# Kernel tuning notes

Measured on AMD Instinct MI355X. Metric: run time of the kernel, lower is better.

Reference implementation:

```python
import jax, jax.numpy as jnp
import numpy as np

B, L, S = 128, 80, 8          # dialogues, utterances per dialogue, speakers
NODE_DIM, HIDDEN, HEADS, OUT_DIM = 768, 512, 8, 256
N = B * L


def _build_edges():
    """Replicates InterSentenceGNN.build_graph + Batch.from_data_list offsets."""
    rel = np.zeros((N, 3), np.float32)
    all_e, last = [], []
    eye3 = np.eye(3, dtype=np.float32)
    for b in range(B):
        off = b * L
        u = L - 1
        e, t = [], []
        for i in range(L):
            if i > 0:
                e += [[i - 1, i], [i, i - 1]]; t += [0, 0]   # REL_SEQ
            if i < u:
                e += [[i, u], [u, i]]; t += [1, 1]           # REL_CTX
        for s in range(S):                                   # REL_SPK, round-robin speakers
            g = list(range(s, L, S))
            for a in range(len(g)):
                for c in range(a + 1, len(g)):
                    e += [[g[a], g[c]], [g[c], g[a]]]; t += [2, 2]
        e = np.asarray(e, np.int64); t = np.asarray(t, np.int64)
        np.add.at(rel, e[:, 0] + off, eye3[t])               # out-degree per relation (pre-unique)
        all_e.append(np.unique(e, axis=0) + off)             # torch.unique(idx, dim=1)
        last.append(off + u)
    edge_index = np.concatenate(all_e, 0).T.astype(np.int32)  # [2, E], row0=src, row1=dst
    return edge_index, rel, np.asarray(last, np.int32)


def setup_inputs() -> dict:
    key = jax.random.key(0)
    ks = jax.random.split(key, 16)
    edge_index, rel_feat, last_idx = _build_edges()
    g = lambda k, shp, fan: jax.random.normal(k, shp, jnp.float32) * (1.0 / np.sqrt(fan))
    return {
        "x": jax.random.normal(ks[0], (N, NODE_DIM), jnp.float32),
        "rel_feat": jnp.asarray(rel_feat),
        "w1": g(ks[1], (3, 64), 3), "b1": jnp.zeros((64,), jnp.float32),
        "w2": g(ks[2], (64, 1), 64), "b2": jnp.zeros((1,), jnp.float32),
        "Wl1": g(ks[3], (NODE_DIM, HIDDEN), NODE_DIM), "bl1": jnp.zeros((HIDDEN,), jnp.float32),
        "Wr1": g(ks[4], (NODE_DIM, HIDDEN), NODE_DIM), "br1": jnp.zeros((HIDDEN,), jnp.float32),
        "att1": g(ks[5], (HEADS, HIDDEN // HEADS), HIDDEN // HEADS),
        "bias1": jnp.zeros((HIDDEN,), jnp.float32),
        "Wl2": g(ks[6], (HIDDEN, OUT_DIM), HIDDEN), "bl2": jnp.zeros((OUT_DIM,), jnp.float32),
        "Wr2": g(ks[7], (HIDDEN, OUT_DIM), HIDDEN), "br2": jnp.zeros((OUT_DIM,), jnp.float32),
        "att2": g(ks[8], (1, OUT_DIM), OUT_DIM),
        "bias2": jnp.zeros((OUT_DIM,), jnp.float32),
        "ln_g": jnp.ones((OUT_DIM,), jnp.float32), "ln_b": jnp.zeros((OUT_DIM,), jnp.float32),
        "edge_index": jnp.asarray(edge_index),
        "last_idx": jnp.asarray(last_idx),
    }


def _gatv2(x, Wl, bl, Wr, br, att, bias, src, dst, heads, ch, concat):
    """PyG GATv2Conv (eval mode, self-loops already in src/dst)."""
    n = x.shape[0]
    xl = (x @ Wl + bl).reshape(n, heads, ch)   # source transform (messages)
    xr = (x @ Wr + br).reshape(n, heads, ch)   # target transform
    e = jax.nn.leaky_relu(xl[src] + xr[dst], negative_slope=0.2)  # [E,H,C]
    logit = jnp.einsum("ehc,hc->eh", e, att)                      # [E,H]
    m = jax.ops.segment_max(logit, dst, num_segments=n)
    a = jnp.exp(logit - m[dst])
    denom = jax.ops.segment_sum(a, dst, num_segments=n)
    alpha = a / denom[dst]                                        # segment softmax over dst
    msg = (xl[src] * alpha[:, :, None]).reshape(-1, heads * ch)
    out = jax.ops.segment_sum(msg, dst, num_segments=n).reshape(n, heads, ch)
    out = out.reshape(n, heads * ch) if concat else out.mean(axis=1)
    return out + bias


def reference(x, rel_feat, w1, b1, w2, b2, Wl1, bl1, Wr1, br1, att1, bias1,
              Wl2, bl2, Wr2, br2, att2, bias2, ln_g, ln_b, edge_index, last_idx):
    n = x.shape[0]
    loops = jnp.arange(n, dtype=edge_index.dtype)
    src = jnp.concatenate([edge_index[0], loops])  # add_self_loops=True (PyG default)
    dst = jnp.concatenate([edge_index[1], loops])
    w = jax.nn.sigmoid(jax.nn.relu(rel_feat @ w1 + b1) @ w2 + b2)  # [N,1] node gate
    h = x * w
    h = jax.nn.elu(_gatv2(h, Wl1, bl1, Wr1, br1, att1, bias1, src, dst, HEADS, HIDDEN // HEADS, True))
    h = _gatv2(h, Wl2, bl2, Wr2, br2, att2, bias2, src, dst, 1, OUT_DIM, False)
    mu = jnp.mean(h, axis=-1, keepdims=True)
    var = jnp.mean((h - mu) ** 2, axis=-1, keepdims=True)
    h = (h - mu) * jax.lax.rsqrt(var + 1e-5) * ln_g + ln_b
    return h[last_idx]  # x[batch.ptr[1:] - 1]: last (context) node per dialogue
```

## Files before the change

kernel.cpp:

```cpp
#include <hip/hip_runtime.h>
#include <hip/hip_bf16.h>

#define NN 10240
#define LL 80
#define BB 128

typedef _Float16 half8 __attribute__((ext_vector_type(8)));
typedef _Float16 half2v __attribute__((ext_vector_type(2)));
typedef float f32x4 __attribute__((ext_vector_type(4)));

#define GLD16(gptr, lptr)                                                        \
  __builtin_amdgcn_global_load_lds(                                              \
      (const __attribute__((address_space(1))) void*)(gptr),                     \
      (__attribute__((address_space(3))) void*)(lptr), 16, 0, 0)

__device__ __forceinline__ float dot2f(half2v a, half2v b, float c) {
#if __has_builtin(__builtin_amdgcn_fdot2)
  return __builtin_amdgcn_fdot2(a, b, c, false);
#else
  return c + (float)a.x * (float)b.x + (float)a.y * (float)b.y;
#endif
}
__device__ __forceinline__ half2v u2h(unsigned int u) { half2v r; __builtin_memcpy(&r, &u, 4); return r; }
__device__ __forceinline__ unsigned int h2u(half2v h) { unsigned int u; __builtin_memcpy(&u, &h, 4); return u; }
__device__ __forceinline__ unsigned int dupf16(float v) {
  _Float16 hv = (_Float16)v;
  unsigned short u; __builtin_memcpy(&u, &hv, 2);
  return (unsigned int)u * 0x10001u;
}
__device__ __forceinline__ int roff(int r) { return r * 66 + 4 * (r >> 3); }

__global__ __launch_bounds__(256) void prep_all(
    const float* __restrict__ x, const float* __restrict__ rel,
    const float* __restrict__ w1, const float* __restrict__ b1,
    const float* __restrict__ w2, const float* __restrict__ b2,
    const float* __restrict__ Wl1, const float* __restrict__ Wr1,
    const float* __restrict__ Wl2, const float* __restrict__ Wr2,
    const float* __restrict__ bl1, const float* __restrict__ br1,
    const float* __restrict__ att1,
    _Float16* __restrict__ h0, _Float16* __restrict__ Wt1,
    _Float16* __restrict__ Wt2cat,
    float* __restrict__ biasc, _Float16* __restrict__ att_h) {
  __shared__ float tile[32][33];
  int bid = blockIdx.x;
  int tid = threadIdx.x;
  if (bid < NN) {
    int n = bid;
    __shared__ float s_w;
    if (tid < 64) {
      float r0 = rel[n * 3 + 0], r1 = rel[n * 3 + 1], r2 = rel[n * 3 + 2];
      float v = r0 * w1[tid] + r1 * w1[64 + tid] + r2 * w1[128 + tid] + b1[tid];
      v = v > 0.f ? v : 0.f;
      v *= w2[tid];
      for (int d = 32; d; d >>= 1) v += __shfl_down(v, d, 64);
      if (tid == 0) s_w = 1.f / (1.f + __expf(-(v + b2[0])));
    }
    __syncthreads();
    float w = s_w;
    const float* xr = x + (size_t)n * 768;
    _Float16* hr = h0 + (size_t)n * 768;
    for (int c = tid; c < 768; c += 256) hr[c] = (_Float16)(xr[c] * w);
    return;
  }
  int r = bid - NN;
  const float* W;
  _Float16* Wt;
  int K, Nc, bx, by;
  if (r < 384)      { W = Wl1; Wt = Wt1;                          K = 768; Nc = 512; bx = r % 16;       by = r / 16; }
  else if (r < 768) { W = Wr1; Wt = Wt1 + (size_t)512 * 768;      K = 768; Nc = 512; bx = (r-384) % 16; by = (r-384) / 16; }
  else if (r < 896) { W = Wl2; Wt = Wt2cat;                       K = 512; Nc = 256; bx = (r-768) % 8;  by = (r-768) / 8; }
  else if (r < 1024){ W = Wr2; Wt = Wt2cat + (size_t)256 * 512;   K = 512; Nc = 256; bx = (r-896) % 8;  by = (r-896) / 8; }
  else {
    for (int i = tid; i < 1024; i += 256) biasc[i] = (i < 512) ? bl1[i] : br1[i - 512];
    for (int i = tid; i < 512; i += 256) att_h[i] = (_Float16)att1[i];
    return;
  }
  int n0 = bx * 32, k0 = by * 32;
  int c = tid & 31, rr = tid >> 5;
#pragma unroll
  for (int p = 0; p < 4; ++p) {
    int rw = p * 8 + rr;
    tile[rw][c] = W[(size_t)(k0 + rw) * Nc + n0 + c];
  }
  __syncthreads();
#pragma unroll
  for (int p = 0; p < 4; ++p) {
    int rw = p * 8 + rr;
    Wt[(size_t)(n0 + rw) * K + k0 + c] = (_Float16)tile[c][rw];
  }
}

__global__ __launch_bounds__(512, 8) void gemm1gat1(
    const _Float16* __restrict__ h0, const _Float16* __restrict__ Wt1,
    const float* __restrict__ biasc, const _Float16* __restrict__ att_h,
    const float* __restrict__ bias1, _Float16* __restrict__ h1) {
  __shared__ __align__(16) char smem[39936];
  _Float16* As = (_Float16*)smem;
  _Float16* Bs = (_Float16*)(smem + 15360);
  _Float16* s_xl = (_Float16*)smem;
  _Float16* s_xr = (_Float16*)(smem + 10640);
  float* s_logit = (float*)(smem + 21280);
  unsigned int* s_al = (unsigned int*)(smem + 26464);
  short* s_src   = (short*)(smem + 31648);
  short* s_cnt   = (short*)(smem + 34240);
  float* s_hub   = (float*)(smem + 34400);
  unsigned int* s_hub16 = (unsigned int*)(smem + 34720);
  unsigned int* s_hp = (unsigned int*)(smem + 35040);

  int bx = blockIdx.x;
  int h = bx >> 7, b = bx & 127;
  int base = b * LL;
  int tid = threadIdx.x;
  int wave = tid >> 6, lane = tid & 63;
  int lr = lane & 15, lk = lane >> 4;

  int seg8 = ((lane & 3) ^ ((lane >> 3) & 3)) * 8;
  const _Float16* aP = h0;
  if (wave < 5) {
    int c = wave * 64 + lane;
    aP = h0 + (size_t)(base + (c >> 2)) * 768 + seg8;
  }
  int cB = wave * 64 + lane;
  int brow = cB >> 2;
  int wrow = (brow < 64) ? (h * 64 + brow) : (512 + h * 64 + (brow - 64));
  const _Float16* bP = Wt1 + (size_t)wrow * 768 + seg8;

  int xk8 = (lk ^ ((lr >> 1) & 3)) * 8;

  f32x4 acc[5] = {};
  for (int it = 0; it < 8; ++it) {
    int k0 = it * 96;
    if (wave < 5) {
      GLD16(aP + k0,      As + wave * 512);
      GLD16(aP + k0 + 32, As + 2560 + wave * 512);
      GLD16(aP + k0 + 64, As + 5120 + wave * 512);
    }
    GLD16(bP + k0,      Bs + wave * 512);
    GLD16(bP + k0 + 32, Bs + 4096 + wave * 512);
    GLD16(bP + k0 + 64, Bs + 8192 + wave * 512);
    __syncthreads();
#pragma unroll
    for (int s3 = 0; s3 < 3; ++s3) {
      half8 bf = *(const half8*)(Bs + s3 * 4096 + (wave * 16 + lr) * 32 + xk8);
#pragma unroll
      for (int m = 0; m < 5; ++m) {
        half8 af = *(const half8*)(As + s3 * 2560 + (m * 16 + lr) * 32 + xk8);
        acc[m] = __builtin_amdgcn_mfma_f32_16x16x32_f16(af, bf, acc[m], 0, 0, 0);
      }
    }
    __syncthreads();
  }
  {
    int c = wave * 16 + lr;
    bool isxl = c < 64;
    int cc = isxl ? c : c - 64;
    float bb = biasc[(isxl ? 0 : 512) + h * 64 + cc];
    _Float16* dst = isxl ? s_xl : s_xr;
#pragma unroll
    for (int m = 0; m < 5; ++m)
#pragma unroll
      for (int rg = 0; rg < 4; ++rg) {
        int row = m * 16 + lk * 4 + rg;
        dst[roff(row) + cc] = (_Float16)(acc[m][rg] + bb);
      }
  }
  if (tid < 79) {
    int d = tid;
    int list[16];
    int c = 0;
    list[c++] = d;
    if (d > 0) list[c++] = d - 1;
    if (d + 1 < 79) list[c++] = d + 1;
    list[c++] = 79;
    for (int j = d & 7; j < 80; j += 8)
      if (j != d && j != 79) list[c++] = j;
    s_cnt[d] = (short)c;
    for (int i = c; i < 16; ++i) list[i] = -1;
#pragma unroll
    for (int i = 0; i < 16; ++i) s_src[i * 81 + d] = (short)list[i];
  }
  __syncthreads();

  const unsigned int* pat = (const unsigned int*)(att_h + h * 64);
  const half2v c02 = {(_Float16)0.2f, (_Float16)0.2f};
  for (int s = tid; s < 1344; s += 512) {
    int d, src;
    bool ishub = s >= 1264;
    if (!ishub) { d = s >> 4; src = s_src[(s & 15) * 81 + d]; }
    else { d = 79; src = s - 1264; }
    int ssrc = src < 0 ? 0 : src;
    const unsigned int* pa = (const unsigned int*)(s_xl + roff(ssrc));
    const unsigned int* pb = (const unsigned int*)(s_xr + roff(d));
    float acc2 = 0.f;
#pragma unroll
    for (int q = 0; q < 16; ++q) {
      unsigned int a0 = pa[2 * q], a1 = pa[2 * q + 1];
      unsigned int b0 = pb[2 * q], b1 = pb[2 * q + 1];
      half2v at0 = u2h(__builtin_amdgcn_readfirstlane(pat[2 * q]));
      half2v at1 = u2h(__builtin_amdgcn_readfirstlane(pat[2 * q + 1]));
      half2v e0 = u2h(a0) + u2h(b0);
      half2v e1 = u2h(a1) + u2h(b1);
      half2v l0 = __builtin_elementwise_max(e0, e0 * c02);
      half2v l1 = __builtin_elementwise_max(e1, e1 * c02);
      acc2 = dot2f(l0, at0, acc2);
      acc2 = dot2f(l1, at1, acc2);
    }
    if (!ishub) s_logit[(s & 15) * 81 + d] = (src < 0) ? -3e38f : acc2;
    else s_hub[src] = acc2;
  }
  __syncthreads();

  if (tid < 79) {
    int d = tid;
    float m = -3e38f, v[16];
#pragma unroll
    for (int i = 0; i < 16; ++i) { v[i] = s_logit[i * 81 + d]; m = fmaxf(m, v[i]); }
    float sum = 0.f;
#pragma unroll
    for (int i = 0; i < 16; ++i) { v[i] = __expf(v[i] - m); sum += v[i]; }
    float inv = 1.f / sum;
#pragma unroll
    for (int i = 0; i < 16; ++i) s_al[i * 81 + d] = dupf16(v[i] * inv);
  } else if (tid >= 448) {
    int l = tid - 448;
    float v0 = s_hub[l];
    float v1 = (l < 16) ? s_hub[64 + l] : -3e38f;
    float m = fmaxf(v0, v1);
    for (int d = 32; d; d >>= 1) m = fmaxf(m, __shfl_xor(m, d, 64));
    float e0 = __expf(v0 - m);
    float e1 = (l < 16) ? __expf(v1 - m) : 0.f;
    float sum = e0 + e1;
    for (int d = 32; d; d >>= 1) sum += __shfl_xor(sum, d, 64);
    float inv = 1.f / sum;
    s_hub16[l] = dupf16(e0 * inv);
    if (l < 16) s_hub16[64 + l] = dupf16(e1 * inv);
  }
  __syncthreads();

  int qw = tid >> 4, l = tid & 15;
  int c0 = l * 4;
#pragma unroll
  for (int k = 0; k < 3; ++k) {
    int d = qw + 32 * k;
    if (d >= 79) continue;
    int cnt = s_cnt[d];
    half2v a0 = {(_Float16)0.f, (_Float16)0.f};
    half2v a1 = a0;
    for (int i = 0; i < cnt; ++i) {
      int src = s_src[i * 81 + d];
      half2v al = u2h(s_al[i * 81 + d]);
      const unsigned int* px = (const unsigned int*)(s_xl + roff(src) + c0);
      a0 += al * u2h(px[0]);
      a1 += al * u2h(px[1]);
    }
    float v0 = (float)a0.x + bias1[h * 64 + c0];
    float v1 = (float)a0.y + bias1[h * 64 + c0 + 1];
    float v2 = (float)a1.x + bias1[h * 64 + c0 + 2];
    float v3 = (float)a1.y + bias1[h * 64 + c0 + 3];
    v0 = v0 > 0.f ? v0 : __expf(v0) - 1.f;
    v1 = v1 > 0.f ? v1 : __expf(v1) - 1.f;
    v2 = v2 > 0.f ? v2 : __expf(v2) - 1.f;
    v3 = v3 > 0.f ? v3 : __expf(v3) - 1.f;
    half2v o0 = {(_Float16)v0, (_Float16)v1};
    half2v o1 = {(_Float16)v2, (_Float16)v3};
    uint2 ov = {h2u(o0), h2u(o1)};
    *(uint2*)&h1[(size_t)(base + d) * 512 + h * 64 + c0] = ov;
  }
  if (qw >= 16) {
    int g = qw - 16;
    half2v a0 = {(_Float16)0.f, (_Float16)0.f};
    half2v a1 = a0;
#pragma unroll
    for (int s5 = 0; s5 < 5; ++s5) {
      int src = g * 5 + s5;
      half2v al = u2h(s_hub16[src]);
      const unsigned int* px = (const unsigned int*)(s_xl + roff(src) + c0);
      a0 += al * u2h(px[0]);
      a1 += al * u2h(px[1]);
    }
    s_hp[g * 32 + 2 * l] = h2u(a0);
    s_hp[g * 32 + 2 * l + 1] = h2u(a1);
  }
  __syncthreads();
  if (tid < 32) {
    float f0 = 0.f, f1 = 0.f;
#pragma unroll
    for (int g = 0; g < 16; ++g) {
      half2v v = u2h(s_hp[g * 32 + tid]);
      f0 += (float)v.x;
      f1 += (float)v.y;
    }
    int c = tid * 2;
    float v0 = f0 + bias1[h * 64 + c];
    float v1 = f1 + bias1[h * 64 + c + 1];
    v0 = v0 > 0.f ? v0 : __expf(v0) - 1.f;
    v1 = v1 > 0.f ? v1 : __expf(v1) - 1.f;
    half2v o = {(_Float16)v0, (_Float16)v1};
    *(unsigned int*)&h1[(size_t)(base + 79) * 512 + h * 64 + c] = h2u(o);
  }
}

#define PX 266
__global__ __launch_bounds__(512) void gemm2gat2(
    const _Float16* __restrict__ h1, const _Float16* __restrict__ Bt,
    const float* __restrict__ bl2, const float* __restrict__ br2,
    const float* __restrict__ att2, const float* __restrict__ bias2,
    const float* __restrict__ ln_g, const float* __restrict__ ln_b,
    float* __restrict__ out) {
  __shared__ __align__(16) char smem[80 * PX * 2];
  __shared__ _Float16 s_att[256];
  __shared__ _Float16 s_xr[256];
  __shared__ float s_red[80];
  __shared__ float s_sum[4], s_sq[4];
  _Float16* As = (_Float16*)smem;
  _Float16* Bs = (_Float16*)(smem + 5120);
  _Float16* s_x = (_Float16*)smem;

  int b = blockIdx.x;
  int tid = threadIdx.x;
  int wave = tid >> 6, lane = tid & 63;
  int lr = lane & 15, lk = lane >> 4;

  if (tid < 256) s_att[tid] = (_Float16)att2[tid];

  int seg8 = ((lane & 3) ^ ((lane >> 3) & 3)) * 8;
  int achunk = wave * 64 + lane;
  const _Float16* aP = h1 + (size_t)(b * 80 + (achunk >> 2)) * 512 + seg8;
  const _Float16* bP[4];
#pragma unroll
  for (int j = 0; j < 4; ++j) {
    int c = wave * 256 + j * 64 + lane;
    bP[j] = Bt + (size_t)(c >> 2) * 512 + seg8;
  }
  int xk8 = (lk ^ ((lr >> 1) & 3)) * 8;
  f32x4 acc[5][4] = {};
  for (int k0 = 0; k0 < 512; k0 += 32) {
    if (wave < 5) GLD16(aP + k0, As + wave * 512);
#pragma unroll
    for (int j = 0; j < 4; ++j)
      GLD16(bP[j] + k0, Bs + (wave * 256 + j * 64) * 8);
    __syncthreads();
    half8 af[5], bfv;
#pragma unroll
    for (int i = 0; i < 5; ++i)
      af[i] = *(const half8*)(As + (i * 16 + lr) * 32 + xk8);
#pragma unroll
    for (int j = 0; j < 4; ++j) {
      bfv = *(const half8*)(Bs + (wave * 64 + j * 16 + lr) * 32 + xk8);
#pragma unroll
      for (int i = 0; i < 5; ++i)
        acc[i][j] = __builtin_amdgcn_mfma_f32_16x16x32_f16(af[i], bfv, acc[i][j], 0, 0, 0);
    }
    __syncthreads();
  }
  if (wave < 4) {
#pragma unroll
    for (int i = 0; i < 5; ++i)
#pragma unroll
      for (int j = 0; j < 4; ++j)
#pragma unroll
        for (int rg = 0; rg < 4; ++rg) {
          int row = i * 16 + lk * 4 + rg;
          int col = wave * 64 + j * 16 + lr;
          s_x[row * PX + col] = (_Float16)(acc[i][j][rg] + bl2[col]);
        }
  } else if (lk == 3) {
#pragma unroll
    for (int j = 0; j < 4; ++j) {
      int colx = (wave - 4) * 64 + j * 16 + lr;
      s_xr[colx] = (_Float16)(acc[4][j][3] + br2[colx]);
    }
  }
  __syncthreads();
  if (tid < 160) {
    int r = tid >> 1, hf = tid & 1;
    const half2v* xa = (const half2v*)(s_x + r * PX + hf * 128);
    const half2v* xr = (const half2v*)(s_xr + hf * 128);
    const half2v* at = (const half2v*)(s_att + hf * 128);
    float lg = 0.f;
    const half2v c02 = {(_Float16)0.2f, (_Float16)0.2f};
#pragma unroll
    for (int q = 0; q < 64; ++q) {
      half2v e = xa[q] + xr[q];
      half2v l = __builtin_elementwise_max(e, e * c02);
      lg = dot2f(l, at[q], lg);
    }
    lg += __shfl_xor(lg, 1, 64);
    if (hf == 0) s_red[r] = lg;
  }
  __syncthreads();
  if (wave == 7) {
    float v0 = s_red[lane];
    float v1 = (lane < 16) ? s_red[64 + lane] : -3e38f;
    float m = fmaxf(v0, v1);
    for (int d = 32; d; d >>= 1) m = fmaxf(m, __shfl_xor(m, d, 64));
    float e0 = __expf(v0 - m);
    float e1 = (lane < 16) ? __expf(v1 - m) : 0.f;
    float sum = e0 + e1;
    for (int d = 32; d; d >>= 1) sum += __shfl_xor(sum, d, 64);
    float inv = 1.f / sum;
    s_red[lane] = e0 * inv;
    if (lane < 16) s_red[64 + lane] = e1 * inv;
  }
  __syncthreads();
  float v = 0.f;
  if (tid < 256) {
    float a = 0.f;
#pragma unroll
    for (int r = 0; r < 80; ++r) a += s_red[r] * (float)s_x[r * PX + tid];
    v = a + bias2[tid];
    float p = v;
    for (int d = 32; d; d >>= 1) p += __shfl_down(p, d, 64);
    if (lane == 0) s_sum[wave] = p;
    float q = v * v;
    for (int d = 32; d; d >>= 1) q += __shfl_down(q, d, 64);
    if (lane == 0) s_sq[wave] = q;
  }
  __syncthreads();
  if (tid < 256) {
    float mu = (s_sum[0] + s_sum[1] + s_sum[2] + s_sum[3]) * (1.f / 256.f);
    float ex2 = (s_sq[0] + s_sq[1] + s_sq[2] + s_sq[3]) * (1.f / 256.f);
    float var = ex2 - mu * mu;
    float r = rsqrtf(var + 1e-5f);
    out[b * 256 + tid] = (v - mu) * r * ln_g[tid] + ln_b[tid];
  }
}

extern "C" void kernel_launch(void* const* d_in, const int* in_sizes, int n_in,
                              void* d_out, int out_size, void* d_ws, size_t ws_size,
                              hipStream_t stream) {
  const float* x      = (const float*)d_in[0];
  const float* rel    = (const float*)d_in[1];
  const float* w1     = (const float*)d_in[2];
  const float* b1     = (const float*)d_in[3];
  const float* w2     = (const float*)d_in[4];
  const float* b2     = (const float*)d_in[5];
  const float* Wl1    = (const float*)d_in[6];
  const float* bl1    = (const float*)d_in[7];
  const float* Wr1    = (const float*)d_in[8];
  const float* br1    = (const float*)d_in[9];
  const float* att1   = (const float*)d_in[10];
  const float* bias1  = (const float*)d_in[11];
  const float* Wl2    = (const float*)d_in[12];
  const float* bl2    = (const float*)d_in[13];
  const float* Wr2    = (const float*)d_in[14];
  const float* br2    = (const float*)d_in[15];
  const float* att2   = (const float*)d_in[16];
  const float* bias2  = (const float*)d_in[17];
  const float* ln_g   = (const float*)d_in[18];
  const float* ln_b   = (const float*)d_in[19];
  float* out = (float*)d_out;

  char* p = (char*)d_ws;
  _Float16* h0     = (_Float16*)p; p += (size_t)NN * 768 * 2;
  _Float16* h1     = (_Float16*)p; p += (size_t)NN * 512 * 2;
  _Float16* Wt1    = (_Float16*)p; p += (size_t)1024 * 768 * 2;
  _Float16* Wt2cat = (_Float16*)p; p += (size_t)512 * 512 * 2;
  _Float16* att_h  = (_Float16*)p; p += 1024;
  float* biasc     = (float*)p; p += 1024 * 4;

  prep_all<<<NN + 1025, 256, 0, stream>>>(x, rel, w1, b1, w2, b2, Wl1, Wr1, Wl2, Wr2,
                                          bl1, br1, att1, h0, Wt1, Wt2cat, biasc, att_h);

  gemm1gat1<<<1024, 512, 0, stream>>>(h0, Wt1, biasc, att_h, bias1, h1);

  gemm2gat2<<<BB, 512, 0, stream>>>(h1, Wt2cat, bl2, br2, att2, bias2, ln_g, ln_b, out);
}
```

Measured before the change: 183.5 us.

## Restructure GAT1 logit computation and drop unused xr GEMM columns in layer 2

```diff
diff --git a/kernel.cpp b/kernel.cpp
--- a/kernel.cpp
+++ b/kernel.cpp
@@ -28,7 +28,21 @@
   unsigned short u; __builtin_memcpy(&u, &hv, 2);
   return (unsigned int)u * 0x10001u;
 }
-__device__ __forceinline__ int roff(int r) { return r * 66 + 4 * (r >> 3); }
+__device__ __forceinline__ int roff(int r) { return r * 72; }
+
+__device__ __forceinline__ float dotq4(uint4 a, uint4 b, const unsigned int* pat, int qb, float acc) {
+  const half2v c02 = {(_Float16)0.2f, (_Float16)0.2f};
+  unsigned int aa[4] = {a.x, a.y, a.z, a.w};
+  unsigned int bb[4] = {b.x, b.y, b.z, b.w};
+#pragma unroll
+  for (int j = 0; j < 4; ++j) {
+    half2v at = u2h(__builtin_amdgcn_readfirstlane(pat[qb + j]));
+    half2v e = u2h(aa[j]) + u2h(bb[j]);
+    half2v l = __builtin_elementwise_max(e, e * c02);
+    acc = dot2f(l, at, acc);
+  }
+  return acc;
+}
 
 __global__ __launch_bounds__(256) void prep_all(
     const float* __restrict__ x, const float* __restrict__ rel,
@@ -98,14 +112,14 @@
   _Float16* As = (_Float16*)smem;
   _Float16* Bs = (_Float16*)(smem + 15360);
   _Float16* s_xl = (_Float16*)smem;
-  _Float16* s_xr = (_Float16*)(smem + 10640);
-  float* s_logit = (float*)(smem + 21280);
-  unsigned int* s_al = (unsigned int*)(smem + 26464);
-  short* s_src   = (short*)(smem + 31648);
-  short* s_cnt   = (short*)(smem + 34240);
-  float* s_hub   = (float*)(smem + 34400);
-  unsigned int* s_hub16 = (unsigned int*)(smem + 34720);
-  unsigned int* s_hp = (unsigned int*)(smem + 35040);
+  _Float16* s_xr = (_Float16*)(smem + 11520);
+  float* s_logit = (float*)(smem + 23040);
+  unsigned int* s_al = (unsigned int*)(smem + 28224);
+  short* s_src   = (short*)(smem + 33408);
+  short* s_cnt   = (short*)(smem + 36000);
+  float* s_hub   = (float*)(smem + 36160);
+  unsigned int* s_hub16 = (unsigned int*)(smem + 36480);
+  unsigned int* s_hp = (unsigned int*)(smem + 36800);
 
   int bx = blockIdx.x;
   int h = bx >> 7, b = bx & 127;
@@ -182,31 +196,45 @@
   __syncthreads();
 
   const unsigned int* pat = (const unsigned int*)(att_h + h * 64);
-  const half2v c02 = {(_Float16)0.2f, (_Float16)0.2f};
-  for (int s = tid; s < 1344; s += 512) {
-    int d, src;
-    bool ishub = s >= 1264;
-    if (!ishub) { d = s >> 4; src = s_src[(s & 15) * 81 + d]; }
-    else { d = 79; src = s - 1264; }
-    int ssrc = src < 0 ? 0 : src;
-    const unsigned int* pa = (const unsigned int*)(s_xl + roff(ssrc));
-    const unsigned int* pb = (const unsigned int*)(s_xr + roff(d));
-    float acc2 = 0.f;
-#pragma unroll
-    for (int q = 0; q < 16; ++q) {
-      unsigned int a0 = pa[2 * q], a1 = pa[2 * q + 1];
-      unsigned int b0 = pb[2 * q], b1 = pb[2 * q + 1];
-      half2v at0 = u2h(__builtin_amdgcn_readfirstlane(pat[2 * q]));
-      half2v at1 = u2h(__builtin_amdgcn_readfirstlane(pat[2 * q + 1]));
-      half2v e0 = u2h(a0) + u2h(b0);
-      half2v e1 = u2h(a1) + u2h(b1);
-      half2v l0 = __builtin_elementwise_max(e0, e0 * c02);
-      half2v l1 = __builtin_elementwise_max(e1, e1 * c02);
-      acc2 = dot2f(l0, at0, acc2);
-      acc2 = dot2f(l1, at1, acc2);
-    }
-    if (!ishub) s_logit[(s & 15) * 81 + d] = (src < 0) ? -3e38f : acc2;
-    else s_hub[src] = acc2;
+  if (tid < 474) {
+    int d = tid / 6, io = tid % 6;
+    const uint4* pxr = (const uint4*)(s_xr + roff(d));
+    uint4 xr[8];
+#pragma unroll
+    for (int q = 0; q < 8; ++q) xr[q] = pxr[q];
+#pragma unroll
+    for (int k = 0; k < 3; ++k) {
+      int i = io + 6 * k;
+      if (i < 16) {
+        int src = s_src[i * 81 + d];
+        if (src < 0) {
+          s_logit[i * 81 + d] = -3e38f;
+        } else {
+          const uint4* pxl = (const uint4*)(s_xl + roff(src));
+          float a2 = 0.f;
+#pragma unroll
+          for (int q = 0; q < 8; ++q) a2 = dotq4(pxl[q], xr[q], pat, q * 4, a2);
+          s_logit[i * 81 + d] = a2;
+        }
+      }
+    }
+  } else {
+    int j = tid - 474;
+    const uint4* pxr = (const uint4*)(s_xr + roff(79));
+    uint4 xr[8];
+#pragma unroll
+    for (int q = 0; q < 8; ++q) xr[q] = pxr[q];
+#pragma unroll
+    for (int k = 0; k < 3; ++k) {
+      int s = j + 38 * k;
+      if (s < 80) {
+        const uint4* pxl = (const uint4*)(s_xl + roff(s));
+        float a2 = 0.f;
+#pragma unroll
+        for (int q = 0; q < 8; ++q) a2 = dotq4(pxl[q], xr[q], pat, q * 4, a2);
+        s_hub[s] = a2;
+      }
+    }
   }
   __syncthreads();
 
@@ -326,50 +354,53 @@
   int seg8 = ((lane & 3) ^ ((lane >> 3) & 3)) * 8;
   int achunk = wave * 64 + lane;
   const _Float16* aP = h1 + (size_t)(b * 80 + (achunk >> 2)) * 512 + seg8;
-  const _Float16* bP[4];
-#pragma unroll
-  for (int j = 0; j < 4; ++j) {
-    int c = wave * 256 + j * 64 + lane;
-    bP[j] = Bt + (size_t)(c >> 2) * 512 + seg8;
-  }
+  const _Float16* bP0 = Bt + (size_t)((wave * 128 + lane) >> 2) * 512 + seg8;
+  const _Float16* bP1 = Bt + (size_t)((wave * 128 + 64 + lane) >> 2) * 512 + seg8;
   int xk8 = (lk ^ ((lr >> 1) & 3)) * 8;
-  f32x4 acc[5][4] = {};
+  f32x4 acc[5][2] = {};
   for (int k0 = 0; k0 < 512; k0 += 32) {
     if (wave < 5) GLD16(aP + k0, As + wave * 512);
-#pragma unroll
-    for (int j = 0; j < 4; ++j)
-      GLD16(bP[j] + k0, Bs + (wave * 256 + j * 64) * 8);
+    GLD16(bP0 + k0, Bs + (wave * 128) * 8);
+    GLD16(bP1 + k0, Bs + (wave * 128 + 64) * 8);
     __syncthreads();
-    half8 af[5], bfv;
+    half8 af[5];
 #pragma unroll
     for (int i = 0; i < 5; ++i)
       af[i] = *(const half8*)(As + (i * 16 + lr) * 32 + xk8);
 #pragma unroll
-    for (int j = 0; j < 4; ++j) {
-      bfv = *(const half8*)(Bs + (wave * 64 + j * 16 + lr) * 32 + xk8);
+    for (int j = 0; j < 2; ++j) {
+      half8 bfv = *(const half8*)(Bs + ((wave * 2 + j) * 16 + lr) * 32 + xk8);
 #pragma unroll
       for (int i = 0; i < 5; ++i)
         acc[i][j] = __builtin_amdgcn_mfma_f32_16x16x32_f16(af[i], bfv, acc[i][j], 0, 0, 0);
     }
     __syncthreads();
   }
-  if (wave < 4) {
-#pragma unroll
-    for (int i = 0; i < 5; ++i)
-#pragma unroll
-      for (int j = 0; j < 4; ++j)
-#pragma unroll
-        for (int rg = 0; rg < 4; ++rg) {
-          int row = i * 16 + lk * 4 + rg;
-          int col = wave * 64 + j * 16 + lr;
-          s_x[row * PX + col] = (_Float16)(acc[i][j][rg] + bl2[col]);
-        }
-  } else if (lk == 3) {
-#pragma unroll
-    for (int j = 0; j < 4; ++j) {
-      int colx = (wave - 4) * 64 + j * 16 + lr;
-      s_xr[colx] = (_Float16)(acc[4][j][3] + br2[colx]);
-    }
+#pragma unroll
+  for (int i = 0; i < 5; ++i)
+#pragma unroll
+    for (int j = 0; j < 2; ++j)
+#pragma unroll
+      for (int rg = 0; rg < 4; ++rg) {
+        int row = i * 16 + lk * 4 + rg;
+        int col = (wave * 2 + j) * 16 + lr;
+        s_x[row * PX + col] = (_Float16)(acc[i][j][rg] + bl2[col]);
+      }
+  {
+    int c = tid >> 1, kh = tid & 1;
+    const uint4* wr = (const uint4*)(Bt + (size_t)(256 + c) * 512 + kh * 256);
+    const uint4* hq = (const uint4*)(h1 + (size_t)(b * 80 + 79) * 512 + kh * 256);
+    float s = 0.f;
+#pragma unroll 8
+    for (int q = 0; q < 32; ++q) {
+      uint4 ua = hq[q], uw = wr[q];
+      s = dot2f(u2h(ua.x), u2h(uw.x), s);
+      s = dot2f(u2h(ua.y), u2h(uw.y), s);
+      s = dot2f(u2h(ua.z), u2h(uw.z), s);
+      s = dot2f(u2h(ua.w), u2h(uw.w), s);
+    }
+    s += __shfl_xor(s, 1, 64);
+    if (kh == 0) s_xr[c] = (_Float16)(s + br2[c]);
   }
   __syncthreads();
   if (tid < 160) {
```

Result: no change. 186.9 us (+1.9%).
